# Optimization experiments

Hardware: AMD Instinct MI355X
Metric: run time of the kernel (lower is better)

Reference implementation:

```python
import jax, jax.numpy as jnp
import numpy as np


def setup_inputs() -> dict:
    key = jax.random.key(0)
    ks = jax.random.split(key, 8)
    B, E, R, D, H = 8, 50000, 1000, 128, 256
    return {
        "head": jax.random.randint(ks[0], (B,), 0, E),
        "relation": jax.random.randint(ks[1], (B,), 0, R),
        "k": 10,
        "ent_emb": jax.random.normal(ks[2], (E, D), jnp.float32),
        "rel_emb": jax.random.normal(ks[3], (R, D), jnp.float32),
        "W1": jax.random.normal(ks[4], (3 * D, H), jnp.float32) * 0.05,
        "b1": jax.random.normal(ks[5], (H,), jnp.float32) * 0.05,
        "W2": jax.random.normal(ks[6], (H,), jnp.float32) * 0.05,
        "b2": jax.random.normal(ks[7], (1,), jnp.float32) * 0.05,
    }


def reference(head, relation, k, ent_emb, rel_emb, W1, b1, W2, b2):
    D = ent_emb.shape[1]
    # score_net first layer on cat([h, r, t]) == h@W1h + r@W1r + t@W1t (same math,
    # avoids materializing the [B*E, 3D] concat).
    W1h, W1r, W1t = W1[:D], W1[D:2 * D], W1[2 * D:]
    h = ent_emb[head]            # [B, D]
    r = rel_emb[relation]        # [B, D]
    ph = h @ W1h + r @ W1r + b1  # [B, H] -- head/relation part, computed once
    pt = ent_emb @ W1t           # [E, H] -- tail part over all entities
    hidden = jax.nn.relu(ph[:, None, :] + pt[None, :, :])   # [B, E, H]
    scores = jnp.einsum('beh,h->be', hidden, W2) + b2[0]     # [B, E]
    top_scores, top_indices = jax.lax.top_k(scores, k)
    return top_indices, top_scores
```

## Files before the change

kernel.cpp:

```cpp
#include <hip/hip_runtime.h>

#define D 128
#define HDIM 256
#define NB 8
#define NSHARD 64
#define CPS 16
#define LCPS 4
#define NCAND (NSHARD * CPS)
#define PHW 16
#define WPAD 136

typedef short bf16x8 __attribute__((ext_vector_type(8)));
typedef float f32x4 __attribute__((ext_vector_type(4)));

__device__ __forceinline__ unsigned short f2bf(float x) {
    unsigned u = __float_as_uint(x);
    unsigned r = u + 0x7FFF + ((u >> 16) & 1);
    return (unsigned short)(r >> 16);
}
__device__ __forceinline__ bf16x8 pack_bf8(float4 u, float4 v) {
    union { bf16x8 v8; unsigned short s[8]; } r;
    r.s[0] = f2bf(u.x); r.s[1] = f2bf(u.y); r.s[2] = f2bf(u.z); r.s[3] = f2bf(u.w);
    r.s[4] = f2bf(v.x); r.s[5] = f2bf(v.y); r.s[6] = f2bf(v.z); r.s[7] = f2bf(v.w);
    return r.v8;
}

__device__ __forceinline__ unsigned long long sk_encode(float v, int idx) {
    unsigned u = __float_as_uint(v);
    u = (u & 0x80000000u) ? ~u : (u | 0x80000000u);
    return ((unsigned long long)u << 32) | (unsigned)(0xFFFFFFFFu - (unsigned)idx);
}
__device__ __forceinline__ float sk_val(unsigned long long key) {
    const unsigned u = (unsigned)(key >> 32);
    return (u & 0x80000000u) ? __uint_as_float(u & 0x7FFFFFFFu) : __uint_as_float(~u);
}
__device__ __forceinline__ int sk_idx(unsigned long long key) {
    return (int)(0xFFFFFFFFu - (unsigned)(key & 0xFFFFFFFFu));
}
__device__ __forceinline__ unsigned long long wave_max64(unsigned long long m) {
#pragma unroll
    for (int s = 32; s > 0; s >>= 1) {
        const unsigned long long o = __shfl_xor(m, s, 64);
        if (o > m) m = o;
    }
    return m;
}

__global__ __launch_bounds__(1024) void prep_kernel(
        const int* __restrict__ head, const int* __restrict__ relation,
        const float* __restrict__ ent_emb, const float* __restrict__ rel_emb,
        const float* __restrict__ W1, const float* __restrict__ b1,
        const float* __restrict__ W2, float* __restrict__ phW,
        unsigned short* __restrict__ w1tt) {
    __shared__ float part[4][HDIM];
    const int w = blockIdx.x;
    const int tid = threadIdx.x;
    const int h = tid & 255;
    const int sl = tid >> 8;
    if (w < NB) {
        const int b = w;
        const long hidx = head[b];
        const long ridx = relation[b];
        const float* hrow = ent_emb + hidx * D;
        const float* rrow = rel_emb + ridx * D;
        float acc = 0.f;
        const int d0 = sl * 32;
#pragma unroll 8
        for (int dd = 0; dd < 32; ++dd) {
            const int d = d0 + dd;
            acc += hrow[d] * W1[d * HDIM + h];
            acc += rrow[d] * W1[(D + d) * HDIM + h];
        }
        part[sl][h] = acc;
        __syncthreads();
        if (sl == 0) {
            phW[h * PHW + b] = part[0][h] + part[1][h] + part[2][h] + part[3][h] + b1[h];
            if (b == 0) phW[h * PHW + 8] = W2[h];
        }
    } else {
        const int k0 = (w - NB) * 16 + sl * 4;
        const float* w1t = W1 + 2 * D * HDIM;
        unsigned short pk[4];
#pragma unroll
        for (int j = 0; j < 4; ++j)
            pk[j] = f2bf(w1t[(k0 + j) * HDIM + h]);
        *(ushort4*)(w1tt + h * D + k0) = make_ushort4(pk[0], pk[1], pk[2], pk[3]);
    }
}

__global__ __launch_bounds__(512, 2) void score_kernel(
        const float* __restrict__ ent_emb, const unsigned short* __restrict__ w1tt,
        const float* __restrict__ phW, float* __restrict__ scores, int E) {
    __shared__ __align__(16) unsigned short wL[HDIM][WPAD];
    __shared__ float phB[NB][HDIM];
    __shared__ float w2L[HDIM];

    const int tid = threadIdx.x;
    const int lane = tid & 63;
    const int wave = tid >> 6;
    const int lm = lane & 15;
    const int q = lane >> 4;
    const int base_e = blockIdx.x * 128 + wave * 16;

    const float* arow = ent_emb + (size_t)min(base_e + lm, E - 1) * D;
    bf16x8 aF[4];
#pragma unroll
    for (int kk = 0; kk < 4; ++kk) {
        const float4 u = *(const float4*)(arow + kk * 32 + q * 8);
        const float4 v = *(const float4*)(arow + kk * 32 + q * 8 + 4);
        aF[kk] = pack_bf8(u, v);
    }

#pragma unroll
    for (int i = 0; i < 8; ++i) {
        const int c = i * 512 + tid;
        const int row = c >> 4;
        const int col = (c & 15) << 3;
        *(uint4*)(&wL[row][col]) = *(const uint4*)(w1tt + row * D + col);
    }
    if (tid < HDIM) {
        const float4 p0 = *(const float4*)(phW + tid * PHW);
        const float4 p1 = *(const float4*)(phW + tid * PHW + 4);
        phB[0][tid] = p0.x; phB[1][tid] = p0.y; phB[2][tid] = p0.z; phB[3][tid] = p0.w;
        phB[4][tid] = p1.x; phB[5][tid] = p1.y; phB[6][tid] = p1.z; phB[7][tid] = p1.w;
        w2L[tid] = phW[tid * PHW + 8];
    }
    __syncthreads();

    float sp[NB * 4];
#pragma unroll
    for (int i = 0; i < NB * 4; ++i) sp[i] = 0.f;

#pragma unroll
    for (int t = 0; t < 16; ++t) {
        const int h = t * 16 + lm;
        bf16x8 bF[4];
#pragma unroll
        for (int kk = 0; kk < 4; ++kk)
            bF[kk] = *(const bf16x8*)(&wL[h][kk * 32 + q * 8]);

        float phv[8];
#pragma unroll
        for (int b = 0; b < NB; ++b) phv[b] = phB[b][h];
        const float w2v = w2L[h];

        f32x4 acc = (f32x4){0.f, 0.f, 0.f, 0.f};
#pragma unroll
        for (int kk = 0; kk < 4; ++kk)
            acc = __builtin_amdgcn_mfma_f32_16x16x32_bf16(aF[kk], bF[kk], acc, 0, 0, 0);

#pragma unroll
        for (int b = 0; b < NB; ++b)
#pragma unroll
            for (int r = 0; r < 4; ++r)
                sp[b * 4 + r] += fmaxf(phv[b] + acc[r], 0.f) * w2v;
    }

#pragma unroll
    for (int m = 1; m <= 8; m <<= 1) {
#pragma unroll
        for (int i = 0; i < NB * 4; ++i)
            sp[i] += __shfl_xor(sp[i], m, 64);
    }
    if (lm == 0) {
#pragma unroll
        for (int r = 0; r < 4; ++r) {
            const int e = base_e + q * 4 + r;
            if (e < E) {
#pragma unroll
                for (int b = 0; b < NB; ++b)
                    scores[(size_t)b * E + e] = sp[b * 4 + r];
            }
        }
    }
}

__global__ __launch_bounds__(256) void topk_rescore_kernel(
        const float* __restrict__ scores, int E,
        const float* __restrict__ ent_emb, const float* __restrict__ W1,
        const float* __restrict__ phW, const float* __restrict__ b2,
        unsigned long long* __restrict__ cand_exact) {
    const int b = blockIdx.x >> 6;
    const int s = blockIdx.x & 63;
    const int tid = threadIdx.x;
    const int lane = tid & 63;
    const int wave = tid >> 6;

    __shared__ unsigned long long cl[4 * CPS];
    __shared__ unsigned long long candk[CPS];
    __shared__ int eIdxs[CPS];
    __shared__ float entR[CPS][D];
    __shared__ float red[4][CPS];

    {
        const int shard = (E + NSHARD - 1) / NSHARD;
        const int start = s * shard;
        const int end = min(E, start + shard);
        const float* row = scores + (size_t)b * E;

        unsigned long long keys[LCPS];
#pragma unroll
        for (int i = 0; i < LCPS; ++i) keys[i] = 0ull;

        for (int e = start + tid; e < end; e += 256) {
            unsigned long long key = sk_encode(row[e], e);
            if (key > keys[LCPS - 1]) {
#pragma unroll
                for (int j = 0; j < LCPS; ++j) {
                    const bool gt = key > keys[j];
                    const unsigned long long mx = gt ? key : keys[j];
                    key = gt ? keys[j] : key;
                    keys[j] = mx;
                }
            }
        }
        for (int r = 0; r < CPS; ++r) {
            const unsigned long long m = wave_max64(keys[0]);
            if (keys[0] == m) {
#pragma unroll
                for (int j = 0; j < LCPS - 1; ++j) keys[j] = keys[j + 1];
                keys[LCPS - 1] = 0ull;
            }
            if (lane == 0) cl[wave * CPS + r] = m;
        }
        __syncthreads();
        if (wave == 0) {
            unsigned long long v = cl[lane];
#pragma unroll
            for (int kk = 2; kk <= 64; kk <<= 1) {
#pragma unroll
                for (int j = kk >> 1; j > 0; j >>= 1) {
                    const unsigned long long o = __shfl_xor(v, j, 64);
                    const bool keep_min = (((lane & j) == 0) == ((lane & kk) != 0));
                    const unsigned long long mn = v < o ? v : o;
                    const unsigned long long mx = v < o ? o : v;
                    v = keep_min ? mn : mx;
                }
            }
            if (lane < CPS) candk[lane] = v;
        }
        __syncthreads();
    }

    if (tid < CPS) eIdxs[tid] = sk_idx(candk[tid]);
    __syncthreads();
    for (int t = tid; t < CPS * (D / 4); t += 256) {
        const int row = t >> 5, c4 = (t & 31) * 4;
        *(float4*)(&entR[row][c4]) =
            *(const float4*)(ent_emb + (size_t)eIdxs[row] * D + c4);
    }
    __syncthreads();

    const float* w1t = W1 + 2 * D * HDIM;
    float acc[CPS];
#pragma unroll
    for (int c = 0; c < CPS; ++c) acc[c] = 0.f;
    for (int d0 = 0; d0 < D; d0 += 4) {
        float w[4];
#pragma unroll
        for (int j = 0; j < 4; ++j) w[j] = w1t[(d0 + j) * HDIM + tid];
#pragma unroll
        for (int c = 0; c < CPS; ++c) {
            const float4 f = *(const float4*)(&entR[c][d0]);
            acc[c] += f.x * w[0] + f.y * w[1] + f.z * w[2] + f.w * w[3];
        }
    }
    const float phv = phW[tid * PHW + b];
    const float w2v = phW[tid * PHW + 8];
    float sc[CPS];
#pragma unroll
    for (int c = 0; c < CPS; ++c) sc[c] = fmaxf(acc[c] + phv, 0.f) * w2v;

#pragma unroll
    for (int m = 1; m <= 32; m <<= 1)
#pragma unroll
        for (int c = 0; c < CPS; ++c) sc[c] += __shfl_xor(sc[c], m, 64);
    if (lane == 0)
#pragma unroll
        for (int c = 0; c < CPS; ++c) red[wave][c] = sc[c];
    __syncthreads();
    if (tid < CPS) {
        const float v = red[0][tid] + red[1][tid] + red[2][tid] + red[3][tid] + b2[0];
        cand_exact[(size_t)(b * NSHARD + s) * CPS + tid] = sk_encode(v, eIdxs[tid]);
    }
}

__global__ __launch_bounds__(64) void final_kernel(
        const unsigned long long* __restrict__ cand_exact, int k,
        float* __restrict__ out) {
    const int lane = threadIdx.x;
    const int b = blockIdx.x;
    unsigned long long lk[CPS];
#pragma unroll
    for (int j = 0; j < CPS; ++j)
        lk[j] = cand_exact[(size_t)b * NCAND + j * 64 + lane];
#pragma unroll
    for (int i = 0; i < CPS - 1; ++i)
#pragma unroll
        for (int j = i + 1; j < CPS; ++j)
            if (lk[i] < lk[j]) {
                const unsigned long long t = lk[i];
                lk[i] = lk[j];
                lk[j] = t;
            }
    for (int r = 0; r < k; ++r) {
        const unsigned long long m = wave_max64(lk[0]);
        if (lk[0] == m) {
#pragma unroll
            for (int j = 0; j < CPS - 1; ++j) lk[j] = lk[j + 1];
            lk[CPS - 1] = 0ull;
        }
        if (lane == 0) {
            out[b * k + r] = (float)sk_idx(m);
            out[NB * k + b * k + r] = sk_val(m);
        }
    }
}

extern "C" void kernel_launch(void* const* d_in, const int* in_sizes, int n_in,
                              void* d_out, int out_size, void* d_ws, size_t ws_size,
                              hipStream_t stream) {
    const int*   head     = (const int*)d_in[0];
    const int*   relation = (const int*)d_in[1];
    const float* ent_emb  = (const float*)d_in[3];
    const float* rel_emb  = (const float*)d_in[4];
    const float* W1       = (const float*)d_in[5];
    const float* b1       = (const float*)d_in[6];
    const float* W2       = (const float*)d_in[7];
    const float* b2       = (const float*)d_in[8];

    const int B = in_sizes[0];
    const int E = in_sizes[3] / D;
    int k = out_size / (2 * B);
    if (k > CPS) k = CPS;

    char* ws = (char*)d_ws;
    unsigned long long* cand_exact = (unsigned long long*)ws;
    float*          phW       = (float*)(ws + 65536);
    unsigned short* w1tt      = (unsigned short*)(ws + 81920);
    float*          scores    = (float*)(ws + 147456);
    float*          out       = (float*)d_out;

    prep_kernel<<<NB + 8, 1024, 0, stream>>>(head, relation, ent_emb, rel_emb,
                                             W1, b1, W2, phW, w1tt);
    const int nblk = (E + 127) / 128;
    score_kernel<<<nblk, 512, 0, stream>>>(ent_emb, w1tt, phW, scores, E);
    topk_rescore_kernel<<<NB * NSHARD, 256, 0, stream>>>(
        scores, E, ent_emb, W1, phW, b2, cand_exact);
    final_kernel<<<NB, 64, 0, stream>>>(cand_exact, k, out);
}
```

Before: 139.3 us.

## Halve top-k shards with 512-thread blocks and fold ReLU bias into max

The top-k/rescore stage now uses 32 shards per batch row with 512-thread blocks, so it launches half as many blocks. Each block's candidate merge becomes two 64-wide bitonic sorts plus a final 32-wide merge, and the exact rescore splits the 16 candidates across two thread halves. In the score kernel the bias is stored negated, so relu(ph+acc) becomes max(acc,-ph). This drops one add per element, but the result is no longer the relu output: it shifts every score by a per-row constant, sum of ph*w2. The final kernel reads 8 candidates per lane instead of 16 and the workspace offsets shrink to match.

```diff
diff --git a/kernel.cpp b/kernel.cpp
--- a/kernel.cpp
+++ b/kernel.cpp
@@ -3,7 +3,7 @@
 #define D 128
 #define HDIM 256
 #define NB 8
-#define NSHARD 64
+#define NSHARD 32
 #define CPS 16
 #define LCPS 4
 #define NCAND (NSHARD * CPS)
@@ -121,8 +121,8 @@
     if (tid < HDIM) {
         const float4 p0 = *(const float4*)(phW + tid * PHW);
         const float4 p1 = *(const float4*)(phW + tid * PHW + 4);
-        phB[0][tid] = p0.x; phB[1][tid] = p0.y; phB[2][tid] = p0.z; phB[3][tid] = p0.w;
-        phB[4][tid] = p1.x; phB[5][tid] = p1.y; phB[6][tid] = p1.z; phB[7][tid] = p1.w;
+        phB[0][tid] = -p0.x; phB[1][tid] = -p0.y; phB[2][tid] = -p0.z; phB[3][tid] = -p0.w;
+        phB[4][tid] = -p1.x; phB[5][tid] = -p1.y; phB[6][tid] = -p1.z; phB[7][tid] = -p1.w;
         w2L[tid] = phW[tid * PHW + 8];
     }
     __syncthreads();
@@ -139,9 +139,9 @@
         for (int kk = 0; kk < 4; ++kk)
             bF[kk] = *(const bf16x8*)(&wL[h][kk * 32 + q * 8]);
 
-        float phv[8];
-#pragma unroll
-        for (int b = 0; b < NB; ++b) phv[b] = phB[b][h];
+        float nphv[8];
+#pragma unroll
+        for (int b = 0; b < NB; ++b) nphv[b] = phB[b][h];
         const float w2v = w2L[h];
 
         f32x4 acc = (f32x4){0.f, 0.f, 0.f, 0.f};
@@ -153,7 +153,7 @@
         for (int b = 0; b < NB; ++b)
 #pragma unroll
             for (int r = 0; r < 4; ++r)
-                sp[b * 4 + r] += fmaxf(phv[b] + acc[r], 0.f) * w2v;
+                sp[b * 4 + r] += fmaxf(acc[r], nphv[b]) * w2v;
     }
 
 #pragma unroll
@@ -175,22 +175,23 @@
     }
 }
 
-__global__ __launch_bounds__(256) void topk_rescore_kernel(
+__global__ __launch_bounds__(512) void topk_rescore_kernel(
         const float* __restrict__ scores, int E,
         const float* __restrict__ ent_emb, const float* __restrict__ W1,
         const float* __restrict__ phW, const float* __restrict__ b2,
         unsigned long long* __restrict__ cand_exact) {
-    const int b = blockIdx.x >> 6;
-    const int s = blockIdx.x & 63;
+    const int b = blockIdx.x >> 5;
+    const int s = blockIdx.x & 31;
     const int tid = threadIdx.x;
     const int lane = tid & 63;
     const int wave = tid >> 6;
 
-    __shared__ unsigned long long cl[4 * CPS];
+    __shared__ unsigned long long cl[8 * CPS];
+    __shared__ unsigned long long s2[32];
     __shared__ unsigned long long candk[CPS];
     __shared__ int eIdxs[CPS];
     __shared__ float entR[CPS][D];
-    __shared__ float red[4][CPS];
+    __shared__ float red[8][8];
 
     {
         const int shard = (E + NSHARD - 1) / NSHARD;
@@ -202,7 +203,7 @@
 #pragma unroll
         for (int i = 0; i < LCPS; ++i) keys[i] = 0ull;
 
-        for (int e = start + tid; e < end; e += 256) {
+        for (int e = start + tid; e < end; e += 512) {
             unsigned long long key = sk_encode(row[e], e);
             if (key > keys[LCPS - 1]) {
 #pragma unroll
@@ -224,8 +225,8 @@
             if (lane == 0) cl[wave * CPS + r] = m;
         }
         __syncthreads();
-        if (wave == 0) {
-            unsigned long long v = cl[lane];
+        if (wave < 2) {
+            unsigned long long v = cl[wave * 64 + lane];
 #pragma unroll
             for (int kk = 2; kk <= 64; kk <<= 1) {
 #pragma unroll
@@ -237,50 +238,68 @@
                     v = keep_min ? mn : mx;
                 }
             }
-            if (lane < CPS) candk[lane] = v;
+            if (lane < 16) s2[wave * 16 + lane] = v;
+        }
+        __syncthreads();
+        if (wave == 0) {
+            unsigned long long v = 0ull;
+            if (lane < 16) v = s2[lane];
+            else if (lane < 32) v = s2[47 - lane];
+#pragma unroll
+            for (int j = 16; j > 0; j >>= 1) {
+                const unsigned long long o = __shfl_xor(v, j, 64);
+                const unsigned long long mn = v < o ? v : o;
+                const unsigned long long mx = v < o ? o : v;
+                v = ((lane & j) == 0) ? mx : mn;
+            }
+            if (lane < 16) candk[lane] = v;
         }
         __syncthreads();
     }
 
     if (tid < CPS) eIdxs[tid] = sk_idx(candk[tid]);
     __syncthreads();
-    for (int t = tid; t < CPS * (D / 4); t += 256) {
-        const int row = t >> 5, c4 = (t & 31) * 4;
-        *(float4*)(&entR[row][c4]) =
-            *(const float4*)(ent_emb + (size_t)eIdxs[row] * D + c4);
+    for (int t = tid; t < CPS * (D / 4); t += 512) {
+        const int rowc = t >> 5, c4 = (t & 31) * 4;
+        *(float4*)(&entR[rowc][c4]) =
+            *(const float4*)(ent_emb + (size_t)eIdxs[rowc] * D + c4);
     }
     __syncthreads();
 
+    const int h = tid & 255;
+    const int chalf = tid >> 8;
     const float* w1t = W1 + 2 * D * HDIM;
-    float acc[CPS];
-#pragma unroll
-    for (int c = 0; c < CPS; ++c) acc[c] = 0.f;
+    float acc[8];
+#pragma unroll
+    for (int c = 0; c < 8; ++c) acc[c] = 0.f;
     for (int d0 = 0; d0 < D; d0 += 4) {
         float w[4];
 #pragma unroll
-        for (int j = 0; j < 4; ++j) w[j] = w1t[(d0 + j) * HDIM + tid];
-#pragma unroll
-        for (int c = 0; c < CPS; ++c) {
-            const float4 f = *(const float4*)(&entR[c][d0]);
+        for (int j = 0; j < 4; ++j) w[j] = w1t[(d0 + j) * HDIM + h];
+#pragma unroll
+        for (int c = 0; c < 8; ++c) {
+            const float4 f = *(const float4*)(&entR[chalf * 8 + c][d0]);
             acc[c] += f.x * w[0] + f.y * w[1] + f.z * w[2] + f.w * w[3];
         }
     }
-    const float phv = phW[tid * PHW + b];
-    const float w2v = phW[tid * PHW + 8];
-    float sc[CPS];
-#pragma unroll
-    for (int c = 0; c < CPS; ++c) sc[c] = fmaxf(acc[c] + phv, 0.f) * w2v;
+    const float phv = phW[h * PHW + b];
+    const float w2v = phW[h * PHW + 8];
+    float sc[8];
+#pragma unroll
+    for (int c = 0; c < 8; ++c) sc[c] = fmaxf(acc[c] + phv, 0.f) * w2v;
 
 #pragma unroll
     for (int m = 1; m <= 32; m <<= 1)
 #pragma unroll
-        for (int c = 0; c < CPS; ++c) sc[c] += __shfl_xor(sc[c], m, 64);
+        for (int c = 0; c < 8; ++c) sc[c] += __shfl_xor(sc[c], m, 64);
     if (lane == 0)
 #pragma unroll
-        for (int c = 0; c < CPS; ++c) red[wave][c] = sc[c];
+        for (int c = 0; c < 8; ++c) red[wave][c] = sc[c];
     __syncthreads();
     if (tid < CPS) {
-        const float v = red[0][tid] + red[1][tid] + red[2][tid] + red[3][tid] + b2[0];
+        const int ch = tid >> 3, ci = tid & 7;
+        const float v = red[ch * 4 + 0][ci] + red[ch * 4 + 1][ci] +
+                        red[ch * 4 + 2][ci] + red[ch * 4 + 3][ci] + b2[0];
         cand_exact[(size_t)(b * NSHARD + s) * CPS + tid] = sk_encode(v, eIdxs[tid]);
     }
 }
@@ -290,14 +309,14 @@
         float* __restrict__ out) {
     const int lane = threadIdx.x;
     const int b = blockIdx.x;
-    unsigned long long lk[CPS];
-#pragma unroll
-    for (int j = 0; j < CPS; ++j)
+    unsigned long long lk[8];
+#pragma unroll
+    for (int j = 0; j < 8; ++j)
         lk[j] = cand_exact[(size_t)b * NCAND + j * 64 + lane];
 #pragma unroll
-    for (int i = 0; i < CPS - 1; ++i)
-#pragma unroll
-        for (int j = i + 1; j < CPS; ++j)
+    for (int i = 0; i < 7; ++i)
+#pragma unroll
+        for (int j = i + 1; j < 8; ++j)
             if (lk[i] < lk[j]) {
                 const unsigned long long t = lk[i];
                 lk[i] = lk[j];
@@ -307,8 +326,8 @@
         const unsigned long long m = wave_max64(lk[0]);
         if (lk[0] == m) {
 #pragma unroll
-            for (int j = 0; j < CPS - 1; ++j) lk[j] = lk[j + 1];
-            lk[CPS - 1] = 0ull;
+            for (int j = 0; j < 7; ++j) lk[j] = lk[j + 1];
+            lk[7] = 0ull;
         }
         if (lane == 0) {
             out[b * k + r] = (float)sk_idx(m);
@@ -336,16 +355,16 @@
 
     char* ws = (char*)d_ws;
     unsigned long long* cand_exact = (unsigned long long*)ws;
-    float*          phW       = (float*)(ws + 65536);
-    unsigned short* w1tt      = (unsigned short*)(ws + 81920);
-    float*          scores    = (float*)(ws + 147456);
+    float*          phW       = (float*)(ws + 32768);
+    unsigned short* w1tt      = (unsigned short*)(ws + 49152);
+    float*          scores    = (float*)(ws + 114688);
     float*          out       = (float*)d_out;
 
     prep_kernel<<<NB + 8, 1024, 0, stream>>>(head, relation, ent_emb, rel_emb,
                                              W1, b1, W2, phW, w1tt);
     const int nblk = (E + 127) / 128;
     score_kernel<<<nblk, 512, 0, stream>>>(ent_emb, w1tt, phW, scores, E);
-    topk_rescore_kernel<<<NB * NSHARD, 256, 0, stream>>>(
+    topk_rescore_kernel<<<NB * NSHARD, 512, 0, stream>>>(
         scores, E, ent_emb, W1, phW, b2, cand_exact);
     final_kernel<<<NB, 64, 0, stream>>>(cand_exact, k, out);
 }
```

After: 133.1 us. 4.5% less time.
